# Performance work log

Hardware: AMD Instinct MI355X
Metric: run time of the kernel (lower is better)

## Reference

```python
import jax, jax.numpy as jnp
import numpy as np

CHANNELS = 3
SCALE = 0.25


def _gaussian_kernel():
    # Mirrors AntiAliasInterpolation2d.__init__
    sigma = (1.0 / SCALE - 1.0) / 2.0            # 1.5
    ka = int(round(sigma * 4))                   # 6 -> kernel_size 13
    k1 = np.exp(-np.arange(-ka, ka + 1, dtype=np.float32) ** 2 / (2.0 * sigma ** 2))
    k2 = np.outer(k1, k1)
    k2 = k2 / k2.sum()
    # depthwise weight: (C_out=C, C_in/groups=1, kh, kw)
    return jnp.asarray(np.tile(k2[None, None], (CHANNELS, 1, 1, 1)).astype(np.float32))


def setup_inputs() -> dict:
    key = jax.random.key(0)
    x = jax.random.normal(key, (32, 3, 512, 512), dtype=jnp.float32)
    weight = _gaussian_kernel()
    return {"x": x, "weight": weight}


def _bilinear_resize(x, out_h, out_w):
    # PyTorch F.interpolate(mode='bilinear', align_corners=False)
    N, C, H, W = x.shape

    def idx(n_in, n_out):
        src = (jnp.arange(n_out, dtype=jnp.float32) + 0.5) * (n_in / n_out) - 0.5
        src = jnp.clip(src, 0.0, n_in - 1)
        i0 = jnp.floor(src).astype(jnp.int32)
        i1 = jnp.minimum(i0 + 1, n_in - 1)
        w = src - i0.astype(jnp.float32)
        return i0, i1, w

    h0, h1, wh = idx(H, out_h)
    w0, w1, ww = idx(W, out_w)
    # interpolate rows then cols
    xh = x[:, :, h0, :] * (1.0 - wh)[:, None] + x[:, :, h1, :] * wh[:, None]
    return xh[:, :, :, w0] * (1.0 - ww) + xh[:, :, :, w1] * ww


def reference(x, weight):
    ka = weight.shape[-1] // 2  # kernel odd -> pad ka on all sides (ka == kb)
    xp = jnp.pad(x, ((0, 0), (0, 0), (ka, ka), (ka, ka)))
    blurred = jax.lax.conv_general_dilated(
        xp, weight,
        window_strides=(1, 1), padding='VALID',
        dimension_numbers=('NCHW', 'OIHW', 'NCHW'),
        feature_group_count=x.shape[1],
    )
    H, W = blurred.shape[2], blurred.shape[3]
    return _bilinear_resize(blurred, int(H * SCALE), int(W * SCALE))
```

## Files before the change

kernel.cpp:

```cpp
#include <hip/hip_runtime.h>
#include <math.h>


#define H 512
#define W 512
#define OH 128
#define OW 128
#define NC 96
#define TAPS 14
#define TI 16
#define NTILES (OH / TI)
#define GRID (NC * NTILES)
#define ROWS (4 * (TI - 1) + TAPS)
#define LSTRIDE (W + W / 32)

typedef float f4 __attribute__((ext_vector_type(4)));

struct G14 { float g[TAPS]; };

__global__ __launch_bounds__(512) void aa_interp_kernel(
    const float* __restrict__ x, float* __restrict__ out, G14 gk) {
    const int bid  = (blockIdx.x & 7) * (GRID / 8) + (blockIdx.x >> 3);
    const int tb   = bid & (NTILES - 1);
    const int nc   = bid >> 3;
    const int t    = threadIdx.x;

    const float* img = x + (size_t)nc * H * W;
    const int r_start = tb * (4 * TI) - 5;

    float acc[TI];
#pragma unroll
    for (int io = 0; io < TI; ++io) acc[io] = 0.f;

    if (tb != 0 && tb != NTILES - 1) {
        const float* p = img + (size_t)r_start * W + t;
#pragma unroll
        for (int k = 0; k < ROWS; ++k) {
            const float v = p[(size_t)k * W];
            const int lo = (k >= TAPS) ? ((k - TAPS + 4) >> 2) : 0;
            const int hi = ((k >> 2) < (TI - 1)) ? (k >> 2) : (TI - 1);
#pragma unroll
            for (int io = lo; io <= hi; ++io) acc[io] += gk.g[k - 4 * io] * v;
        }
    } else {
#pragma unroll
        for (int k = 0; k < ROWS; ++k) {
            const int r = r_start + k;
            float v = 0.f;
            if (r >= 0 && r < H) v = img[(size_t)r * W + t];
            const int lo = (k >= TAPS) ? ((k - TAPS + 4) >> 2) : 0;
            const int hi = ((k >> 2) < (TI - 1)) ? (k >> 2) : (TI - 1);
#pragma unroll
            for (int io = lo; io <= hi; ++io) acc[io] += gk.g[k - 4 * io] * v;
        }
    }

    __shared__ float lds[TI * LSTRIDE];
    {
        const int a = t + (t >> 5);
#pragma unroll
        for (int io = 0; io < TI; ++io) lds[io * LSTRIDE + a] = acc[io];
    }
    __syncthreads();

    const int io = t >> 5;
    const int jg = t & 31;
    const int j0 = jg * 4;
    const float* lrow = lds + io * LSTRIDE;
    const int cb = 4 * j0 - 5;

    float win[26];
#pragma unroll
    for (int w = 0; w < 26; ++w) {
        const int c = cb + w;
        float v = 0.f;
        if (c >= 0 && c < W) v = lrow[c + (c >> 5)];
        win[w] = v;
    }

    f4 res;
#pragma unroll
    for (int jj = 0; jj < 4; ++jj) {
        float s = 0.f;
#pragma unroll
        for (int v = 0; v < TAPS; ++v) s += gk.g[v] * win[4 * jj + v];
        res[jj] = s;
    }

    float* op = out + ((size_t)nc * OH + tb * TI + io) * OW + j0;
    __builtin_nontemporal_store(res, (f4*)op);
}

extern "C" void kernel_launch(void* const* d_in, const int* in_sizes, int n_in,
                              void* d_out, int out_size, void* d_ws, size_t ws_size,
                              hipStream_t stream) {
    const float* x = (const float*)d_in[0];
    float* out = (float*)d_out;

    G14 gk;
    {
        double k1[13], s = 0.0;
        for (int d = 0; d < 13; ++d) {
            double dd = d - 6;
            k1[d] = exp(-(dd * dd) / (2.0 * 1.5 * 1.5));
            s += k1[d];
        }
        for (int u = 0; u < TAPS; ++u) {
            double lo = (u - 1 >= 0 && u - 1 < 13) ? k1[u - 1] : 0.0;
            double hi = (u < 13) ? k1[u] : 0.0;
            gk.g[u] = (float)(0.5 * (lo + hi) / s);
        }
    }

    aa_interp_kernel<<<GRID, 512, 0, stream>>>(x, out, gk);
}
```

Baseline: 22.64 us.

## Split vertical pass by row parity across thread halves with float2 loads

Each thread now handles two adjacent columns, loaded as float2. The two halves of the block process even and odd input rows separately, and their partial sums are combined in LDS through an extra barrier. The boundary fast path is dropped, so every load is bounds-checked, launch bounds gain an occupancy hint, and the output store becomes a normal store instead of a nontemporal one. This aims at wider memory transactions and shorter per-thread dependency chains, at the cost of more registers, an extra sync and a read-modify-write pass in LDS.

```diff
diff --git a/kernel.cpp b/kernel.cpp
--- a/kernel.cpp
+++ b/kernel.cpp
@@ -12,54 +12,81 @@
 #define NTILES (OH / TI)
 #define GRID (NC * NTILES)
 #define ROWS (4 * (TI - 1) + TAPS)
+#define NPAIRS (ROWS / 2)
 #define LSTRIDE (W + W / 32)
 
 typedef float f4 __attribute__((ext_vector_type(4)));
 
 struct G14 { float g[TAPS]; };
 
-__global__ __launch_bounds__(512) void aa_interp_kernel(
+__global__ __launch_bounds__(512, 6) void aa_interp_kernel(
     const float* __restrict__ x, float* __restrict__ out, G14 gk) {
     const int bid  = (blockIdx.x & 7) * (GRID / 8) + (blockIdx.x >> 3);
     const int tb   = bid & (NTILES - 1);
     const int nc   = bid >> 3;
     const int t    = threadIdx.x;
+    const int half = t >> 8;
+    const int tc   = t & 255;
 
-    const float* img = x + (size_t)nc * H * W;
+    const float* img  = x + (size_t)nc * H * W;
+    const float* colp = img + 2 * tc;
     const int r_start = tb * (4 * TI) - 5;
 
-    float acc[TI];
+    float acc[TI][2];
 #pragma unroll
-    for (int io = 0; io < TI; ++io) acc[io] = 0.f;
+    for (int io = 0; io < TI; ++io) { acc[io][0] = 0.f; acc[io][1] = 0.f; }
 
-    if (tb != 0 && tb != NTILES - 1) {
-        const float* p = img + (size_t)r_start * W + t;
+    if (half == 0) {
 #pragma unroll
-        for (int k = 0; k < ROWS; ++k) {
-            const float v = p[(size_t)k * W];
+        for (int m = 0; m < NPAIRS; ++m) {
+            const int k = 2 * m;
+            const int r = r_start + k;
+            float2 v = make_float2(0.f, 0.f);
+            if (r >= 0 && r < H) v = *reinterpret_cast<const float2*>(colp + (size_t)r * W);
             const int lo = (k >= TAPS) ? ((k - TAPS + 4) >> 2) : 0;
             const int hi = ((k >> 2) < (TI - 1)) ? (k >> 2) : (TI - 1);
 #pragma unroll
-            for (int io = lo; io <= hi; ++io) acc[io] += gk.g[k - 4 * io] * v;
+            for (int io = lo; io <= hi; ++io) {
+                const float g = gk.g[k - 4 * io];
+                acc[io][0] += g * v.x;
+                acc[io][1] += g * v.y;
+            }
         }
     } else {
 #pragma unroll
-        for (int k = 0; k < ROWS; ++k) {
+        for (int m = 0; m < NPAIRS; ++m) {
+            const int k = 2 * m + 1;
             const int r = r_start + k;
-            float v = 0.f;
-            if (r >= 0 && r < H) v = img[(size_t)r * W + t];
+            float2 v = make_float2(0.f, 0.f);
+            if (r >= 0 && r < H) v = *reinterpret_cast<const float2*>(colp + (size_t)r * W);
             const int lo = (k >= TAPS) ? ((k - TAPS + 4) >> 2) : 0;
             const int hi = ((k >> 2) < (TI - 1)) ? (k >> 2) : (TI - 1);
 #pragma unroll
-            for (int io = lo; io <= hi; ++io) acc[io] += gk.g[k - 4 * io] * v;
+            for (int io = lo; io <= hi; ++io) {
+                const float g = gk.g[k - 4 * io];
+                acc[io][0] += g * v.x;
+                acc[io][1] += g * v.y;
+            }
         }
     }
 
     __shared__ float lds[TI * LSTRIDE];
-    {
-        const int a = t + (t >> 5);
+    const int c0 = 2 * tc;
+    const int a0 = c0 + (c0 >> 5);
+    if (half == 1) {
 #pragma unroll
-        for (int io = 0; io < TI; ++io) lds[io * LSTRIDE + a] = acc[io];
+        for (int io = 0; io < TI; ++io) {
+            lds[io * LSTRIDE + a0]     = acc[io][0];
+            lds[io * LSTRIDE + a0 + 1] = acc[io][1];
+        }
+    }
+    __syncthreads();
+    if (half == 0) {
+#pragma unroll
+        for (int io = 0; io < TI; ++io) {
+            lds[io * LSTRIDE + a0]     += acc[io][0];
+            lds[io * LSTRIDE + a0 + 1] += acc[io][1];
+        }
     }
     __syncthreads();
 
@@ -88,7 +115,7 @@
     }
 
     float* op = out + ((size_t)nc * OH + tb * TI + io) * OW + j0;
-    __builtin_nontemporal_store(res, (f4*)op);
+    *reinterpret_cast<f4*>(op) = res;
 }
 
 extern "C" void kernel_launch(void* const* d_in, const int* in_sizes, int n_in,
```

Result: no change. 22.22 us (-1.8%).
